# Kernel tuning notes

Measured on AMD Instinct MI355X. Metric: run time of the kernel, lower is better.

## Reference

```python
import jax, jax.numpy as jnp
import numpy as np

B, S, D, H = 2, 2048, 1024, 16
HD = D // H  # 64


def setup_inputs() -> dict:
    key = jax.random.key(0)
    ks = jax.random.split(key, 7)
    s = 1.0 / np.sqrt(HD)
    return {
        "x": jax.random.normal(ks[0], (B, S, D), dtype=jnp.float32),
        "Wq": jax.random.normal(ks[1], (H, HD, HD), dtype=jnp.float32) * s,
        "bq": jax.random.normal(ks[2], (H, HD), dtype=jnp.float32) * 0.01,
        "Wk": jax.random.normal(ks[3], (H, HD, HD), dtype=jnp.float32) * s,
        "bk": jax.random.normal(ks[4], (H, HD), dtype=jnp.float32) * 0.01,
        "Wv": jax.random.normal(ks[5], (H, HD, HD), dtype=jnp.float32) * s,
        "bv": jax.random.normal(ks[6], (H, HD), dtype=jnp.float32) * 0.01,
    }


def reference(x, Wq, bq, Wk, bk, Wv, bv):
    b, s, d = x.shape
    h, hd, _ = Wq.shape
    # Faithful to torch: x.view(B, H, S, hd) is a raw reshape (mixes seq positions
    # across heads), NOT a transpose-based head split.
    xh = x.reshape(b, h, s, hd)
    # torch Linear: y @ W.T + b, with W of shape (out, in)
    q = jnp.einsum('bhse,hde->bhsd', xh, Wq) + bq[None, :, None, :]
    k = jnp.einsum('bhse,hde->bhsd', xh, Wk) + bk[None, :, None, :]
    v = jnp.einsum('bhse,hde->bhsd', xh, Wv) + bv[None, :, None, :]
    scale = 1.0 / jnp.sqrt(jnp.asarray(d / h, dtype=jnp.float32))
    attn = jax.nn.softmax(jnp.einsum('bhqd,bhkd->bhqk', q, k) * scale, axis=-1)
    out = jnp.einsum('bhqk,bhkd->bhqd', attn, v)
    # torch.cat over heads along last dim == transpose then merge
    return out.transpose(0, 2, 1, 3).reshape(b, s, d)
```

## Files before the change

### kernel.cpp

```cpp
#include <hip/hip_runtime.h>
#include <hip/hip_bf16.h>

#define BATCH 2
#define SEQ   2048
#define DMODEL 1024
#define NH    16
#define HD    64
#define QSCALE 0.1803368801111602f

typedef __attribute__((ext_vector_type(8))) short bf16x8;
typedef __attribute__((ext_vector_type(4))) float f32x4;

__device__ __forceinline__ ushort f2bf(float f) {
    union { float f; unsigned u; } v; v.f = f;
    return (ushort)((v.u + 0x8000u) >> 16);
}

__device__ __forceinline__ unsigned pack2bf(float a, float b) {
    union { float f; unsigned u; } x, y; x.f = a; y.f = b;
    return __builtin_amdgcn_perm(y.u + 0x8000u, x.u + 0x8000u, 0x07060302u);
}

__device__ __forceinline__ float exp2r(float x) {
#if __has_builtin(__builtin_amdgcn_exp2f)
    return __builtin_amdgcn_exp2f(x);
#else
    return exp2f(x);
#endif
}

#define MFMA(a, b, c) __builtin_amdgcn_mfma_f32_16x16x32_bf16((a), (b), (c), 0, 0, 0)

__global__ __launch_bounds__(256) void qkv_kernel(
    const float* __restrict__ x,
    const float* __restrict__ Wq, const float* __restrict__ bq,
    const float* __restrict__ Wk, const float* __restrict__ bk,
    const float* __restrict__ Wv, const float* __restrict__ bv,
    ushort* __restrict__ Qo, ushort* __restrict__ Kf, ushort* __restrict__ Vf)
{
    const int bid = blockIdx.x;
    const int ch  = bid & 7;
    const int bh  = bid >> 3;
    const int h   = bh & (NH - 1);

    __shared__ ushort Xs[64 * 72];
    __shared__ ushort Ws[3 * 64 * 72];

    const int tid  = threadIdx.x;
    const int wave = tid >> 6, lane = tid & 63;
    const int ln16 = lane & 15, quad = lane >> 4;

    const float* wsrc[3] = { Wq + h * 4096, Wk + h * 4096, Wv + h * 4096 };
    for (int m = 0; m < 3; ++m)
        for (int i = 0; i < 4; ++i) {
            int idx = tid + 256 * i;
            float4 v = ((const float4*)wsrc[m])[idx];
            if (m == 0) { v.x *= QSCALE; v.y *= QSCALE; v.z *= QSCALE; v.w *= QSCALE; }
            int row = idx >> 4, c4 = (idx & 15) * 4;
            ushort4 o;
            o.x = f2bf(v.x); o.y = f2bf(v.y); o.z = f2bf(v.z); o.w = f2bf(v.w);
            *(ushort4*)&Ws[m * 64 * 72 + row * 72 + c4] = o;
        }

    const float* bias[3] = { bq + h * 64, bk + h * 64, bv + h * 64 };
    ushort* Eb = Xs;

    for (int tt = 0; tt < 4; ++tt) {
        const int st = ch * 4 + tt;
        __syncthreads();

        const float* xp = x + (size_t)bh * (SEQ * HD) + (size_t)st * 64 * HD;
        for (int i = 0; i < 4; ++i) {
            int idx = tid + 256 * i;
            float4 v = ((const float4*)xp)[idx];
            int row = idx >> 4, c4 = (idx & 15) * 4;
            ushort4 o;
            o.x = f2bf(v.x); o.y = f2bf(v.y); o.z = f2bf(v.z); o.w = f2bf(v.w);
            *(ushort4*)&Xs[row * 72 + c4] = o;
        }
        __syncthreads();

        bf16x8 afr[2];
        for (int ks = 0; ks < 2; ++ks)
            afr[ks] = *(const bf16x8*)&Xs[(wave * 16 + ln16) * 72 + ks * 32 + quad * 8];
        __syncthreads();

        for (int m = 0; m < 3; ++m) {
            f32x4 acc[4];
            for (int nt = 0; nt < 4; ++nt) {
                acc[nt] = (f32x4){0.f, 0.f, 0.f, 0.f};
                for (int ks = 0; ks < 2; ++ks) {
                    bf16x8 bfr = *(const bf16x8*)&Ws[m * 64 * 72 + (nt * 16 + ln16) * 72 + ks * 32 + quad * 8];
                    acc[nt] = MFMA(afr[ks], bfr, acc[nt]);
                }
            }
            if (m < 2) {
                for (int nt = 0; nt < 4; ++nt) {
                    float bb = bias[m][nt * 16 + ln16];
                    if (m == 0) bb *= QSCALE;
                    for (int r = 0; r < 4; ++r)
                        Eb[(wave * 16 + quad * 4 + r) * 72 + nt * 16 + ln16] = f2bf(acc[nt][r] + bb);
                }
                __syncthreads();
                if (m == 0) {
                    ushort* dst = Qo + (size_t)bh * SEQ * HD + (size_t)st * 64 * HD;
                    for (int i = 0; i < 2; ++i) {
                        int idx = tid + 256 * i;
                        int row = idx >> 3, c8 = (idx & 7) * 8;
                        *(bf16x8*)&dst[row * 64 + c8] = *(const bf16x8*)&Eb[row * 72 + c8];
                    }
                } else {
                    ushort* dst = Kf + ((size_t)bh * 32 + st) * 4096;
                    for (int i = 0; i < 2; ++i) {
                        int idx8 = tid + 256 * i;
                        int l2 = idx8 & 63, chunk = idx8 >> 6;
                        int nt = chunk >> 1, ks = chunk & 1;
                        int qd = l2 >> 4, l16 = l2 & 15;
                        *(bf16x8*)&dst[(size_t)idx8 * 8] =
                            *(const bf16x8*)&Eb[(nt * 16 + l16) * 72 + ks * 32 + qd * 8];
                    }
                }
                __syncthreads();
            } else {
                for (int nt = 0; nt < 4; ++nt) {
                    float bb = bias[2][nt * 16 + ln16];
                    ushort4 o;
                    o.x = f2bf(acc[nt][0] + bb);
                    o.y = f2bf(acc[nt][1] + bb);
                    o.z = f2bf(acc[nt][2] + bb);
                    o.w = f2bf(acc[nt][3] + bb);
                    *(ushort4*)&Eb[(nt * 16 + ln16) * 72 + wave * 16 + quad * 4] = o;
                }
                __syncthreads();
                ushort* dst = Vf + ((size_t)bh * 32 + st) * 4096;
                for (int i = 0; i < 2; ++i) {
                    int idx8 = tid + 256 * i;
                    int l2 = idx8 & 63, chunk = idx8 >> 6;
                    int nt = chunk >> 1, ks = chunk & 1;
                    int qd = l2 >> 4, l16 = l2 & 15;
                    *(bf16x8*)&dst[(size_t)idx8 * 8] =
                        *(const bf16x8*)&Eb[(nt * 16 + l16) * 72 + ks * 32 + qd * 8];
                }
            }
        }
    }
}

__global__ __launch_bounds__(256, 2) void attn_kernel(
    const ushort* __restrict__ Q, const ushort* __restrict__ Kf,
    const ushort* __restrict__ Vf, float* __restrict__ out)
{
    const int bid = blockIdx.x;
    const int qt  = bid & 15;
    const int bh  = bid >> 4;
    const int h   = bh & (NH - 1), b = bh >> 4;

    __shared__ ushort Ps[4][2][32 * 72];

    const int tid = threadIdx.x, wave = tid >> 6, lane = tid & 63;
    const int ln16 = lane & 15, quad = lane >> 4;

    bf16x8 qfr[2][2];
#pragma unroll
    for (int g = 0; g < 2; ++g) {
        const ushort* Qg = Q + ((size_t)bh * SEQ + qt * 128 + wave * 32 + g * 16 + ln16) * HD;
        qfr[g][0] = *(const bf16x8*)&Qg[quad * 8];
        qfr[g][1] = *(const bf16x8*)&Qg[32 + quad * 8];
    }

    const bf16x8* kfp = (const bf16x8*)(Kf + (size_t)bh * 32 * 4096) + lane;
    const bf16x8* vfp = (const bf16x8*)(Vf + (size_t)bh * 32 * 4096) + lane;

    float lsum[2] = {0.f, 0.f};
    f32x4 accO[2][4];
#pragma unroll
    for (int g = 0; g < 2; ++g)
#pragma unroll
        for (int nt = 0; nt < 4; ++nt) accO[g][nt] = (f32x4){0.f, 0.f, 0.f, 0.f};

    bf16x8 kf[8], vf[8];
#pragma unroll
    for (int c = 0; c < 8; ++c) kf[c] = kfp[c * 64];
    kfp += 512;

    for (int kt = 0; kt < 32; ++kt) {
        const int cur = kt & 1;

        f32x4 sacc[2][4];
#pragma unroll
        for (int nt = 0; nt < 4; ++nt)
#pragma unroll
            for (int g = 0; g < 2; ++g) {
                f32x4 a = {0.f, 0.f, 0.f, 0.f};
                a = MFMA(kf[nt * 2],     qfr[g][0], a);
                a = MFMA(kf[nt * 2 + 1], qfr[g][1], a);
                sacc[g][nt] = a;
            }

        if (kt < 31) {
#pragma unroll
            for (int c = 0; c < 8; ++c) kf[c] = kfp[c * 64];
            kfp += 512;
        }

        if (kt > 0) {
            const ushort* Pr = Ps[wave][1 - cur];
            bf16x8 pf[2][2];
#pragma unroll
            for (int g = 0; g < 2; ++g) {
                pf[g][0] = *(const bf16x8*)&Pr[(g * 16 + ln16) * 72 + quad * 8];
                pf[g][1] = *(const bf16x8*)&Pr[(g * 16 + ln16) * 72 + 32 + quad * 8];
            }
#pragma unroll
            for (int nt = 0; nt < 4; ++nt)
#pragma unroll
                for (int g = 0; g < 2; ++g) {
                    accO[g][nt] = MFMA(vf[nt * 2],     pf[g][0], accO[g][nt]);
                    accO[g][nt] = MFMA(vf[nt * 2 + 1], pf[g][1], accO[g][nt]);
                }
        }

#pragma unroll
        for (int c = 0; c < 8; ++c) vf[c] = vfp[c * 64];
        vfp += 512;

        ushort* Pw = Ps[wave][cur];
#pragma unroll
        for (int g = 0; g < 2; ++g) {
            float rs = 0.f;
#pragma unroll
            for (int nt = 0; nt < 4; ++nt) {
                float p0 = exp2r(sacc[g][nt][0]);
                float p1 = exp2r(sacc[g][nt][1]);
                float p2 = exp2r(sacc[g][nt][2]);
                float p3 = exp2r(sacc[g][nt][3]);
                rs += (p0 + p1) + (p2 + p3);
                uint2 pk;
                pk.x = pack2bf(p0, p1);
                pk.y = pack2bf(p2, p3);
                *(uint2*)&Pw[(g * 16 + ln16) * 72 + nt * 16 + quad * 4] = pk;
            }
            lsum[g] += rs;
        }
    }

    {
        const ushort* Pr = Ps[wave][31 & 1];
        bf16x8 pf[2][2];
#pragma unroll
        for (int g = 0; g < 2; ++g) {
            pf[g][0] = *(const bf16x8*)&Pr[(g * 16 + ln16) * 72 + quad * 8];
            pf[g][1] = *(const bf16x8*)&Pr[(g * 16 + ln16) * 72 + 32 + quad * 8];
        }
#pragma unroll
        for (int nt = 0; nt < 4; ++nt)
#pragma unroll
            for (int g = 0; g < 2; ++g) {
                accO[g][nt] = MFMA(vf[nt * 2],     pf[g][0], accO[g][nt]);
                accO[g][nt] = MFMA(vf[nt * 2 + 1], pf[g][1], accO[g][nt]);
            }
    }

#pragma unroll
    for (int g = 0; g < 2; ++g) {
        float l = lsum[g];
        l += __shfl_xor(l, 16, 64);
        l += __shfl_xor(l, 32, 64);
        float rinv = 1.0f / l;
        float* ob = out + ((size_t)b * SEQ + qt * 128 + wave * 32 + g * 16 + ln16) * DMODEL + h * HD;
#pragma unroll
        for (int nt = 0; nt < 4; ++nt) {
            float4 o;
            o.x = accO[g][nt][0] * rinv;
            o.y = accO[g][nt][1] * rinv;
            o.z = accO[g][nt][2] * rinv;
            o.w = accO[g][nt][3] * rinv;
            *(float4*)&ob[nt * 16 + quad * 4] = o;
        }
    }
}

extern "C" void kernel_launch(void* const* d_in, const int* in_sizes, int n_in,
                              void* d_out, int out_size, void* d_ws, size_t ws_size,
                              hipStream_t stream) {
    const float* x  = (const float*)d_in[0];
    const float* Wq = (const float*)d_in[1];
    const float* bq = (const float*)d_in[2];
    const float* Wk = (const float*)d_in[3];
    const float* bk = (const float*)d_in[4];
    const float* Wv = (const float*)d_in[5];
    const float* bv = (const float*)d_in[6];

    const size_t nElem = (size_t)BATCH * NH * SEQ * HD;
    ushort* Qw = (ushort*)d_ws;
    ushort* Kw = Qw + nElem;
    ushort* Vw = Kw + nElem;

    qkv_kernel<<<32 * 8, 256, 0, stream>>>(
        x, Wq, bq, Wk, bk, Wv, bv, Qw, Kw, Vw);
    attn_kernel<<<BATCH * NH * (SEQ / 128), 256, 0, stream>>>(
        Qw, Kw, Vw, (float*)d_out);
}
```

Before: 128.4 us.

## Shrink attention blocks, compute row sums via MFMA, truncate P to bf16

The attention kernel now uses 128-thread blocks covering 64 queries, which doubles the grid. The QKV kernel also gets twice as many blocks, each handling half the sequence tiles. The softmax row sum is no longer built from scalar adds and cross-lane shuffles; an extra MFMA against a ones vector accumulates it from the bf16 P values. P is packed by truncation instead of rounding, and the P fragment loads from LDS are hoisted ahead of the QK MFMAs. Together these aim to improve occupancy and overlap and to cut VALU work, at the cost of more K/V re-reads across blocks and a few extra MFMAs per tile.

```diff
diff --git a/kernel.cpp b/kernel.cpp
--- a/kernel.cpp
+++ b/kernel.cpp
@@ -16,9 +16,9 @@
     return (ushort)((v.u + 0x8000u) >> 16);
 }
 
-__device__ __forceinline__ unsigned pack2bf(float a, float b) {
+__device__ __forceinline__ unsigned pack2bf_t(float a, float b) {
     union { float f; unsigned u; } x, y; x.f = a; y.f = b;
-    return __builtin_amdgcn_perm(y.u + 0x8000u, x.u + 0x8000u, 0x07060302u);
+    return __builtin_amdgcn_perm(y.u, x.u, 0x07060302u);
 }
 
 __device__ __forceinline__ float exp2r(float x) {
@@ -39,8 +39,8 @@
     ushort* __restrict__ Qo, ushort* __restrict__ Kf, ushort* __restrict__ Vf)
 {
     const int bid = blockIdx.x;
-    const int ch  = bid & 7;
-    const int bh  = bid >> 3;
+    const int ch  = bid & 15;
+    const int bh  = bid >> 4;
     const int h   = bh & (NH - 1);
 
     __shared__ ushort Xs[64 * 72];
@@ -65,8 +65,8 @@
     const float* bias[3] = { bq + h * 64, bk + h * 64, bv + h * 64 };
     ushort* Eb = Xs;
 
-    for (int tt = 0; tt < 4; ++tt) {
-        const int st = ch * 4 + tt;
+    for (int tt = 0; tt < 2; ++tt) {
+        const int st = ch * 2 + tt;
         __syncthreads();
 
         const float* xp = x + (size_t)bh * (SEQ * HD) + (size_t)st * 64 * HD;
@@ -146,16 +146,16 @@
     }
 }
 
-__global__ __launch_bounds__(256, 2) void attn_kernel(
+__global__ __launch_bounds__(128, 2) void attn_kernel(
     const ushort* __restrict__ Q, const ushort* __restrict__ Kf,
     const ushort* __restrict__ Vf, float* __restrict__ out)
 {
     const int bid = blockIdx.x;
-    const int qt  = bid & 15;
-    const int bh  = bid >> 4;
+    const int qt  = bid & 31;
+    const int bh  = bid >> 5;
     const int h   = bh & (NH - 1), b = bh >> 4;
 
-    __shared__ ushort Ps[4][2][32 * 72];
+    __shared__ ushort Ps[2][2][32 * 72];
 
     const int tid = threadIdx.x, wave = tid >> 6, lane = tid & 63;
     const int ln16 = lane & 15, quad = lane >> 4;
@@ -163,7 +163,7 @@
     bf16x8 qfr[2][2];
 #pragma unroll
     for (int g = 0; g < 2; ++g) {
-        const ushort* Qg = Q + ((size_t)bh * SEQ + qt * 128 + wave * 32 + g * 16 + ln16) * HD;
+        const ushort* Qg = Q + ((size_t)bh * SEQ + qt * 64 + wave * 32 + g * 16 + ln16) * HD;
         qfr[g][0] = *(const bf16x8*)&Qg[quad * 8];
         qfr[g][1] = *(const bf16x8*)&Qg[32 + quad * 8];
     }
@@ -171,12 +171,17 @@
     const bf16x8* kfp = (const bf16x8*)(Kf + (size_t)bh * 32 * 4096) + lane;
     const bf16x8* vfp = (const bf16x8*)(Vf + (size_t)bh * 32 * 4096) + lane;
 
-    float lsum[2] = {0.f, 0.f};
-    f32x4 accO[2][4];
-#pragma unroll
-    for (int g = 0; g < 2; ++g)
+    bf16x8 ones;
+#pragma unroll
+    for (int j = 0; j < 8; ++j) ones[j] = (short)0x3F80;
+
+    f32x4 accO[2][4], accL[2];
+#pragma unroll
+    for (int g = 0; g < 2; ++g) {
+        accL[g] = (f32x4){0.f, 0.f, 0.f, 0.f};
 #pragma unroll
         for (int nt = 0; nt < 4; ++nt) accO[g][nt] = (f32x4){0.f, 0.f, 0.f, 0.f};
+    }
 
     bf16x8 kf[8], vf[8];
 #pragma unroll
@@ -185,6 +190,16 @@
 
     for (int kt = 0; kt < 32; ++kt) {
         const int cur = kt & 1;
+
+        bf16x8 pf[2][2];
+        if (kt > 0) {
+            const ushort* Pr = Ps[wave][1 - cur];
+#pragma unroll
+            for (int g = 0; g < 2; ++g) {
+                pf[g][0] = *(const bf16x8*)&Pr[(g * 16 + ln16) * 72 + quad * 8];
+                pf[g][1] = *(const bf16x8*)&Pr[(g * 16 + ln16) * 72 + 32 + quad * 8];
+            }
+        }
 
         f32x4 sacc[2][4];
 #pragma unroll
@@ -204,13 +219,6 @@
         }
 
         if (kt > 0) {
-            const ushort* Pr = Ps[wave][1 - cur];
-            bf16x8 pf[2][2];
-#pragma unroll
-            for (int g = 0; g < 2; ++g) {
-                pf[g][0] = *(const bf16x8*)&Pr[(g * 16 + ln16) * 72 + quad * 8];
-                pf[g][1] = *(const bf16x8*)&Pr[(g * 16 + ln16) * 72 + 32 + quad * 8];
-            }
 #pragma unroll
             for (int nt = 0; nt < 4; ++nt)
 #pragma unroll
@@ -218,6 +226,11 @@
                     accO[g][nt] = MFMA(vf[nt * 2],     pf[g][0], accO[g][nt]);
                     accO[g][nt] = MFMA(vf[nt * 2 + 1], pf[g][1], accO[g][nt]);
                 }
+#pragma unroll
+            for (int g = 0; g < 2; ++g) {
+                accL[g] = MFMA(ones, pf[g][0], accL[g]);
+                accL[g] = MFMA(ones, pf[g][1], accL[g]);
+            }
         }
 
 #pragma unroll
@@ -226,26 +239,22 @@
 
         ushort* Pw = Ps[wave][cur];
 #pragma unroll
-        for (int g = 0; g < 2; ++g) {
-            float rs = 0.f;
+        for (int g = 0; g < 2; ++g)
 #pragma unroll
             for (int nt = 0; nt < 4; ++nt) {
                 float p0 = exp2r(sacc[g][nt][0]);
                 float p1 = exp2r(sacc[g][nt][1]);
                 float p2 = exp2r(sacc[g][nt][2]);
                 float p3 = exp2r(sacc[g][nt][3]);
-                rs += (p0 + p1) + (p2 + p3);
                 uint2 pk;
-                pk.x = pack2bf(p0, p1);
-                pk.y = pack2bf(p2, p3);
+                pk.x = pack2bf_t(p0, p1);
+                pk.y = pack2bf_t(p2, p3);
                 *(uint2*)&Pw[(g * 16 + ln16) * 72 + nt * 16 + quad * 4] = pk;
             }
-            lsum[g] += rs;
-        }
     }
 
     {
-        const ushort* Pr = Ps[wave][31 & 1];
+        const ushort* Pr = Ps[wave][1];
         bf16x8 pf[2][2];
 #pragma unroll
         for (int g = 0; g < 2; ++g) {
@@ -259,15 +268,17 @@
                 accO[g][nt] = MFMA(vf[nt * 2],     pf[g][0], accO[g][nt]);
                 accO[g][nt] = MFMA(vf[nt * 2 + 1], pf[g][1], accO[g][nt]);
             }
+#pragma unroll
+        for (int g = 0; g < 2; ++g) {
+            accL[g] = MFMA(ones, pf[g][0], accL[g]);
+            accL[g] = MFMA(ones, pf[g][1], accL[g]);
+        }
     }
 
 #pragma unroll
     for (int g = 0; g < 2; ++g) {
-        float l = lsum[g];
-        l += __shfl_xor(l, 16, 64);
-        l += __shfl_xor(l, 32, 64);
-        float rinv = 1.0f / l;
-        float* ob = out + ((size_t)b * SEQ + qt * 128 + wave * 32 + g * 16 + ln16) * DMODEL + h * HD;
+        float rinv = 1.0f / accL[g][0];
+        float* ob = out + ((size_t)b * SEQ + qt * 64 + wave * 32 + g * 16 + ln16) * DMODEL + h * HD;
 #pragma unroll
         for (int nt = 0; nt < 4; ++nt) {
             float4 o;
@@ -296,8 +307,8 @@
     ushort* Kw = Qw + nElem;
     ushort* Vw = Kw + nElem;
 
-    qkv_kernel<<<32 * 8, 256, 0, stream>>>(
+    qkv_kernel<<<32 * 16, 256, 0, stream>>>(
         x, Wq, bq, Wk, bk, Wv, bv, Qw, Kw, Vw);
-    attn_kernel<<<BATCH * NH * (SEQ / 128), 256, 0, stream>>>(
+    attn_kernel<<<BATCH * NH * (SEQ / 64), 128, 0, stream>>>(
         Qw, Kw, Vw, (float*)d_out);
 }
```

Result: no change. 129.6 us (+1.0%).

## Split attention key range across two wave groups and double QKV grid

Applied to the files above, without the earlier changes.

The attention kernel now launches 512 threads per block. Two halves of the waves each process half of the key tiles for the same query rows, and their partial outputs and row sums are combined through shared memory at the end. This is possible because the softmax here needs no running max. The QKV projection grid is doubled, with each block handling two sequence tiles instead of four, and the P-fragment LDS reads are hoisted ahead of the score MFMAs. The aim is more waves in flight to hide the latency of global K/V loads, at the cost of a cross-half reduction, a larger shared buffer and higher register pressure from launch_bounds(512,4).

```diff
diff --git a/kernel.cpp b/kernel.cpp
--- a/kernel.cpp
+++ b/kernel.cpp
@@ -39,8 +39,8 @@
     ushort* __restrict__ Qo, ushort* __restrict__ Kf, ushort* __restrict__ Vf)
 {
     const int bid = blockIdx.x;
-    const int ch  = bid & 7;
-    const int bh  = bid >> 3;
+    const int ch  = bid & 15;
+    const int bh  = bid >> 4;
     const int h   = bh & (NH - 1);
 
     __shared__ ushort Xs[64 * 72];
@@ -65,8 +65,8 @@
     const float* bias[3] = { bq + h * 64, bk + h * 64, bv + h * 64 };
     ushort* Eb = Xs;
 
-    for (int tt = 0; tt < 4; ++tt) {
-        const int st = ch * 4 + tt;
+    for (int tt = 0; tt < 2; ++tt) {
+        const int st = ch * 2 + tt;
         __syncthreads();
 
         const float* xp = x + (size_t)bh * (SEQ * HD) + (size_t)st * 64 * HD;
@@ -146,7 +146,7 @@
     }
 }
 
-__global__ __launch_bounds__(256, 2) void attn_kernel(
+__global__ __launch_bounds__(512, 4) void attn_kernel(
     const ushort* __restrict__ Q, const ushort* __restrict__ Kf,
     const ushort* __restrict__ Vf, float* __restrict__ out)
 {
@@ -155,62 +155,66 @@
     const int bh  = bid >> 4;
     const int h   = bh & (NH - 1), b = bh >> 4;
 
-    __shared__ ushort Ps[4][2][32 * 72];
+    __shared__ ushort Ps[8][2][32 * 72];
 
     const int tid = threadIdx.x, wave = tid >> 6, lane = tid & 63;
+    const int half = wave >> 2, w4 = wave & 3;
     const int ln16 = lane & 15, quad = lane >> 4;
 
     bf16x8 qfr[2][2];
 #pragma unroll
     for (int g = 0; g < 2; ++g) {
-        const ushort* Qg = Q + ((size_t)bh * SEQ + qt * 128 + wave * 32 + g * 16 + ln16) * HD;
+        const ushort* Qg = Q + ((size_t)bh * SEQ + qt * 128 + w4 * 32 + g * 16 + ln16) * HD;
         qfr[g][0] = *(const bf16x8*)&Qg[quad * 8];
         qfr[g][1] = *(const bf16x8*)&Qg[32 + quad * 8];
     }
 
-    const bf16x8* kfp = (const bf16x8*)(Kf + (size_t)bh * 32 * 4096) + lane;
-    const bf16x8* vfp = (const bf16x8*)(Vf + (size_t)bh * 32 * 4096) + lane;
-
+    const bf16x8* kfp = (const bf16x8*)(Kf + ((size_t)bh * 32 + half * 16) * 4096) + lane;
+    const bf16x8* vfp = (const bf16x8*)(Vf + ((size_t)bh * 32 + half * 16) * 4096) + lane;
+
+    const f32x4 fz = {0.f, 0.f, 0.f, 0.f};
     float lsum[2] = {0.f, 0.f};
     f32x4 accO[2][4];
 #pragma unroll
     for (int g = 0; g < 2; ++g)
 #pragma unroll
-        for (int nt = 0; nt < 4; ++nt) accO[g][nt] = (f32x4){0.f, 0.f, 0.f, 0.f};
+        for (int nt = 0; nt < 4; ++nt) accO[g][nt] = fz;
 
     bf16x8 kf[8], vf[8];
 #pragma unroll
     for (int c = 0; c < 8; ++c) kf[c] = kfp[c * 64];
     kfp += 512;
 
-    for (int kt = 0; kt < 32; ++kt) {
+    for (int kt = 0; kt < 16; ++kt) {
         const int cur = kt & 1;
 
-        f32x4 sacc[2][4];
-#pragma unroll
-        for (int nt = 0; nt < 4; ++nt)
-#pragma unroll
-            for (int g = 0; g < 2; ++g) {
-                f32x4 a = {0.f, 0.f, 0.f, 0.f};
-                a = MFMA(kf[nt * 2],     qfr[g][0], a);
-                a = MFMA(kf[nt * 2 + 1], qfr[g][1], a);
-                sacc[g][nt] = a;
-            }
-
-        if (kt < 31) {
-#pragma unroll
-            for (int c = 0; c < 8; ++c) kf[c] = kfp[c * 64];
-            kfp += 512;
-        }
-
+        bf16x8 pf[2][2];
         if (kt > 0) {
             const ushort* Pr = Ps[wave][1 - cur];
-            bf16x8 pf[2][2];
 #pragma unroll
             for (int g = 0; g < 2; ++g) {
                 pf[g][0] = *(const bf16x8*)&Pr[(g * 16 + ln16) * 72 + quad * 8];
                 pf[g][1] = *(const bf16x8*)&Pr[(g * 16 + ln16) * 72 + 32 + quad * 8];
             }
+        }
+
+        f32x4 sacc[2][4];
+#pragma unroll
+        for (int nt = 0; nt < 4; ++nt)
+#pragma unroll
+            for (int g = 0; g < 2; ++g) {
+                f32x4 a = MFMA(kf[nt * 2], qfr[g][0], fz);
+                a = MFMA(kf[nt * 2 + 1], qfr[g][1], a);
+                sacc[g][nt] = a;
+            }
+
+        if (kt < 15) {
+#pragma unroll
+            for (int c = 0; c < 8; ++c) kf[c] = kfp[c * 64];
+            kfp += 512;
+        }
+
+        if (kt > 0) {
 #pragma unroll
             for (int nt = 0; nt < 4; ++nt)
 #pragma unroll
@@ -245,7 +249,7 @@
     }
 
     {
-        const ushort* Pr = Ps[wave][31 & 1];
+        const ushort* Pr = Ps[wave][1];
         bf16x8 pf[2][2];
 #pragma unroll
         for (int g = 0; g < 2; ++g) {
@@ -263,19 +267,41 @@
 
 #pragma unroll
     for (int g = 0; g < 2; ++g) {
-        float l = lsum[g];
-        l += __shfl_xor(l, 16, 64);
-        l += __shfl_xor(l, 32, 64);
-        float rinv = 1.0f / l;
-        float* ob = out + ((size_t)b * SEQ + qt * 128 + wave * 32 + g * 16 + ln16) * DMODEL + h * HD;
-#pragma unroll
-        for (int nt = 0; nt < 4; ++nt) {
-            float4 o;
-            o.x = accO[g][nt][0] * rinv;
-            o.y = accO[g][nt][1] * rinv;
-            o.z = accO[g][nt][2] * rinv;
-            o.w = accO[g][nt][3] * rinv;
-            *(float4*)&ob[nt * 16 + quad * 4] = o;
+        lsum[g] += __shfl_xor(lsum[g], 16, 64);
+        lsum[g] += __shfl_xor(lsum[g], 32, 64);
+    }
+
+    __syncthreads();
+    float* cb = (float*)&Ps[0][0][0];
+    float* lb = cb + 128 * 68;
+    if (half == 1) {
+#pragma unroll
+        for (int g = 0; g < 2; ++g) {
+            int row = w4 * 32 + g * 16 + ln16;
+#pragma unroll
+            for (int nt = 0; nt < 4; ++nt)
+                *(f32x4*)&cb[row * 68 + nt * 16 + quad * 4] = accO[g][nt];
+            if (quad == 0) lb[row] = lsum[g];
+        }
+    }
+    __syncthreads();
+    if (half == 0) {
+#pragma unroll
+        for (int g = 0; g < 2; ++g) {
+            int row = w4 * 32 + g * 16 + ln16;
+            float l = lsum[g] + lb[row];
+            float rinv = 1.0f / l;
+            float* ob = out + ((size_t)b * SEQ + qt * 128 + row) * DMODEL + h * HD;
+#pragma unroll
+            for (int nt = 0; nt < 4; ++nt) {
+                f32x4 part = *(const f32x4*)&cb[row * 68 + nt * 16 + quad * 4];
+                float4 o;
+                o.x = (accO[g][nt][0] + part[0]) * rinv;
+                o.y = (accO[g][nt][1] + part[1]) * rinv;
+                o.z = (accO[g][nt][2] + part[2]) * rinv;
+                o.w = (accO[g][nt][3] + part[3]) * rinv;
+                *(float4*)&ob[nt * 16 + quad * 4] = o;
+            }
         }
     }
 }
@@ -296,8 +322,8 @@
     ushort* Kw = Qw + nElem;
     ushort* Vw = Kw + nElem;
 
-    qkv_kernel<<<32 * 8, 256, 0, stream>>>(
+    qkv_kernel<<<32 * 16, 256, 0, stream>>>(
         x, Wq, bq, Wk, bk, Wv, bv, Qw, Kw, Vw);
-    attn_kernel<<<BATCH * NH * (SEQ / 128), 256, 0, stream>>>(
+    attn_kernel<<<BATCH * NH * (SEQ / 128), 512, 0, stream>>>(
         Qw, Kw, Vw, (float*)d_out);
 }
```

After: 148.1 us. 1.15x slower.
